# Kernel tuning notes

Hardware: AMD Instinct MI355X
Metric: run time of the kernel (lower is better)

The kernel has to match this reference:

```python
import jax, jax.numpy as jnp
import numpy as np

D_MODEL = 2048
D_STATE = 64
D_HEAD = 64
EXPAND = 2
CHUNK = 256
D_INNER = EXPAND * D_MODEL          # 4096
N_HEADS = D_INNER // D_HEAD          # 64
PARAM_DIM = 1 + 2 * D_STATE          # 129


def setup_inputs() -> dict:
    key = jax.random.key(0)
    k0, k1, k2, k3 = jax.random.split(key, 4)
    x = jax.random.normal(k0, (1, 4096, D_MODEL), jnp.float32)
    w_in = jax.random.normal(k1, (2 * D_INNER, D_MODEL), jnp.float32) * 0.02
    w_param = jax.random.normal(k2, (N_HEADS * PARAM_DIM, D_MODEL), jnp.float32) * 0.02
    w_out = jax.random.normal(k3, (D_MODEL, D_INNER), jnp.float32) * 0.02
    return {"x": x, "w_in": w_in, "w_param": w_param, "w_out": w_out}


def _ssd(a, Bm, Cm, X, Q):
    # a: (nb, l), Bm/Cm: (nb, l, ds), X: (nb, l, dh). Mamba-2 SSD chunked scan.
    nb, l = a.shape
    ds = Bm.shape[-1]
    dh = X.shape[-1]
    nc = l // Q
    la = jnp.log(a).reshape(nb, nc, Q)
    cs = jnp.cumsum(la, axis=-1)                      # cumulative log-decay within chunk
    Bc = Bm.reshape(nb, nc, Q, ds)
    Cc = Cm.reshape(nb, nc, Q, ds)
    Xc = X.reshape(nb, nc, Q, dh)
    # intra-chunk (attention-like dual): L[i,j] = prod_{r=j+1..i} a_r, j<=i
    tri = jnp.tril(jnp.ones((Q, Q), bool))
    L = jnp.where(tri, jnp.exp(cs[..., :, None] - cs[..., None, :]), 0.0)
    scores = jnp.einsum('znid,znjd->znij', Cc, Bc) * L
    y_diag = jnp.einsum('znij,znjh->znih', scores, Xc)
    # per-chunk state contribution: sum_j decay_to_end[j] * B_j^T x_j -> (nb,nc,ds,dh)
    decay_states = jnp.exp(cs[..., -1:] - cs)
    states = jnp.einsum('znj,znjd,znjh->zndh', decay_states, Bc, Xc)
    A_chunk = jnp.exp(cs[..., -1])                    # total decay per chunk (nb, nc)
    def step(S, inp):
        Ac, st = inp
        S_prev = S
        return Ac[:, None, None] * S + st, S_prev
    S0 = jnp.zeros((nb, ds, dh), a.dtype)
    _, S_prev = jax.lax.scan(step, S0, (A_chunk.T, jnp.moveaxis(states, 1, 0)))
    S_prev = jnp.moveaxis(S_prev, 0, 1)               # state entering each chunk (nb,nc,ds,dh)
    y_inter = jnp.einsum('znid,zndh,zni->znih', Cc, S_prev, jnp.exp(cs))
    return (y_diag + y_inter).reshape(nb, l, dh)


def reference(x, w_in, w_param, w_out):
    b, l, _ = x.shape
    xr = x @ w_in.T                                   # (b, l, 2*d_inner)
    inp, res = xr[..., :D_INNER], xr[..., D_INNER:]
    params = (x @ w_param.T).reshape(b, l, N_HEADS, PARAM_DIM)
    dt = jax.nn.softplus(params[..., 0])
    a = jnp.exp(-dt)                                  # (b, l, n_heads)
    Bp = params[..., 1:1 + D_STATE]
    Cp = params[..., 1 + D_STATE:]
    nb = b * N_HEADS
    # NOTE: raw row-major reshapes, mirroring the torch source exactly
    y = _ssd(a.reshape(nb, l),
             Bp.reshape(nb, l, D_STATE),
             Cp.reshape(nb, l, D_STATE),
             inp.reshape(nb, l, D_HEAD),
             CHUNK)
    y = y.reshape(b, l, D_INNER)
    out = y * jax.nn.silu(res)
    return out @ w_out.T
```

## Files before the change

kernel.cpp:

```cpp
#include <hip/hip_runtime.h>
#include <math.h>

#define Q 256

typedef unsigned short u16;
typedef unsigned int u32;
typedef __attribute__((ext_vector_type(8))) short short8;
typedef __attribute__((ext_vector_type(4))) float f32x4;

__device__ __forceinline__ float bf2f(u32 u){
  union { float f; u32 i; } v; v.i = u << 16; return v.f;
}
__device__ __forceinline__ u16 f2bf(float f){
  union { float f; u32 i; } v; v.f = f;
  u32 r = (v.i + 0x7FFFu + ((v.i >> 16) & 1u)) >> 16;
  return (u16)r;
}
__device__ __forceinline__ float softplusf(float x){
  return x > 20.f ? x : log1pf(expf(x));
}
__device__ __forceinline__ float siluf(float x){
  return x / (1.f + expf(-x));
}

__device__ __forceinline__ void gload_lds16(const void* g, const void* l){
  __builtin_amdgcn_global_load_lds(
    (const __attribute__((address_space(1))) void*)(uintptr_t)g,
    (__attribute__((address_space(3))) void*)(u32)(uintptr_t)l,
    16, 0, 0);
}

__device__ __forceinline__ u32 swz_off(int row, int col2){
  return (u32)(row*128 + (col2 ^ ((row & 7) << 4)));
}
__device__ __forceinline__ short8 frag_ld(const u16* buf, int row, int kk, int lk){
  return *(const short8*)((const char*)buf + row*128 + (((kk*4 + lk) ^ (row & 7)) << 4));
}

__global__ __launch_bounds__(256) void cast_bf16(const float* __restrict__ in,
    u16* __restrict__ out)
{
  const size_t i = ((size_t)blockIdx.x * 256 + threadIdx.x) * 4;
  const float4 v = *(const float4*)(in + i);
  ushort4 o;
  o.x = f2bf(v.x); o.y = f2bf(v.y); o.z = f2bf(v.z); o.w = f2bf(v.w);
  *(ushort4*)(out + i) = o;
}

#define G256_VM8 asm volatile("s_waitcnt vmcnt(8)" ::: "memory")
#define G256_VM4 asm volatile("s_waitcnt vmcnt(4)" ::: "memory")
#define G256_VM0 asm volatile("s_waitcnt vmcnt(0)" ::: "memory")

#define G256_STAGE(s_) \
  _Pragma("unroll") for (int q = 0; q < 4; q++) \
    gload_lds16(sptr[q] + (s_)*32, lds + (((s_)&3)*32768) + (q*512 + tid)*16);

#define G256_PHASE(p_, dostage_, VMSTMT) { \
  const char* sb_ = lds + (((p_)&3)*32768); \
  short8 af_[8], bf_[4]; \
  _Pragma("unroll") for (int m = 0; m < 8; m++) af_[m] = *(const short8*)(sb_ + aoff[m]); \
  _Pragma("unroll") for (int n = 0; n < 4; n++) bf_[n] = *(const short8*)(sb_ + boff[n]); \
  if (dostage_) { G256_STAGE((p_)+3) } \
  __builtin_amdgcn_s_barrier(); \
  asm volatile("s_waitcnt lgkmcnt(0)" ::: "memory"); \
  __builtin_amdgcn_sched_barrier(0); \
  __builtin_amdgcn_s_setprio(1); \
  _Pragma("unroll") for (int m = 0; m < 8; m++) \
  _Pragma("unroll") for (int n = 0; n < 4; n++) \
    acc[m][n] = __builtin_amdgcn_mfma_f32_16x16x32_bf16(af_[m], bf_[n], acc[m][n], 0, 0, 0); \
  __builtin_amdgcn_s_setprio(0); \
  VMSTMT; \
  __builtin_amdgcn_s_barrier(); \
}

#define G256_CORE(A_, B_, K_, NTN_) \
  extern __shared__ char lds[]; \
  const int tid = threadIdx.x; \
  const int nwg = gridDim.x, bid = blockIdx.x; \
  const int wg = (bid & 7) * (nwg >> 3) + (bid >> 3); \
  const int m0 = (wg / (NTN_)) * 256, n0 = (wg % (NTN_)) * 256; \
  const int w = tid >> 6, l = tid & 63; \
  const int wr = w >> 2, wc = w & 3; \
  const int lr = l & 15, lk = l >> 4; \
  const u16* sptr[4]; \
  _Pragma("unroll") for (int q = 0; q < 4; q++) { \
    const int c = q*512 + tid; \
    const int r = c >> 3; \
    const int jl = (c & 7) ^ (r & 7); \
    sptr[q] = (jl < 4) ? ((A_) + (size_t)(m0 + r)*(K_) + jl*8) \
                       : ((B_) + (size_t)(n0 + r)*(K_) + (jl-4)*8); \
  } \
  int aoff[8], boff[4]; \
  _Pragma("unroll") for (int m = 0; m < 8; m++) { \
    const int r = wr*128 + m*16 + lr; \
    aoff[m] = r*128 + ((lk ^ (r & 7)) << 4); } \
  _Pragma("unroll") for (int n = 0; n < 4; n++) { \
    const int r = wc*64 + n*16 + lr; \
    boff[n] = r*128 + (((4 + lk) ^ (r & 7)) << 4); } \
  f32x4 acc[8][4]; \
  { f32x4 z = {0.f,0.f,0.f,0.f}; \
    _Pragma("unroll") for (int m = 0; m < 8; m++) \
    _Pragma("unroll") for (int n = 0; n < 4; n++) acc[m][n] = z; } \
  G256_STAGE(0) G256_STAGE(1) G256_STAGE(2) \
  G256_VM8; \
  __builtin_amdgcn_s_barrier(); \
  { const int NPH = (K_)/32; \
    for (int p = 0; p < NPH-4; p += 4) { \
      G256_PHASE(p,   1, G256_VM8) \
      G256_PHASE(p+1, 1, G256_VM8) \
      G256_PHASE(p+2, 1, G256_VM8) \
      G256_PHASE(p+3, 1, G256_VM8) \
    } \
    G256_PHASE(NPH-4, 1, G256_VM8) \
    G256_PHASE(NPH-3, 0, G256_VM4) \
    G256_PHASE(NPH-2, 0, G256_VM0) \
    G256_PHASE(NPH-1, 0, (void)0) \
  }

__global__ void __launch_bounds__(512, 2) gemm_in256(const u16* __restrict__ A,
    const u16* __restrict__ B, u16* __restrict__ inp, u16* __restrict__ resb)
{
  G256_CORE(A, B, 2048, 32)
  #pragma unroll
  for (int m = 0; m < 8; m++)
    #pragma unroll
    for (int n = 0; n < 4; n++) {
      const int col = n0 + wc*64 + n*16 + lr;
      #pragma unroll
      for (int j = 0; j < 4; j++) {
        const int row = m0 + wr*128 + m*16 + lk*4 + j;
        const u16 v = f2bf(acc[m][n][j]);
        if (col < 4096) inp[(size_t)row*4096 + col] = v;
        else            resb[(size_t)row*4096 + (col - 4096)] = v;
      }
    }
}

__global__ void __launch_bounds__(512, 2) gemm_par256(const u16* __restrict__ A,
    const u16* __restrict__ B, float* __restrict__ dtb,
    u16* __restrict__ Bb, u16* __restrict__ Cb)
{
  G256_CORE(A, B, 2048, 33)
  #pragma unroll
  for (int m = 0; m < 8; m++)
    #pragma unroll
    for (int n = 0; n < 4; n++) {
      const int col = n0 + wc*64 + n*16 + lr;
      if (col < 8256) {
        const int h = col / 129, rr = col - h*129;
        #pragma unroll
        for (int j = 0; j < 4; j++) {
          const int row = m0 + wr*128 + m*16 + lk*4 + j;
          const float v = acc[m][n][j];
          if (rr == 0)      dtb[(size_t)row*64 + h] = v;
          else if (rr < 65) Bb[((size_t)row*64 + h)*64 + (rr-1)]  = f2bf(v);
          else              Cb[((size_t)row*64 + h)*64 + (rr-65)] = f2bf(v);
        }
      }
    }
}

#define MFMA_GEMM_CORE(Abf_, Bbf_, K_) \
  __shared__ short As[128*64]; \
  __shared__ short Bs[128*64]; \
  const int tid = threadIdx.x; \
  const int w = tid >> 6, l = tid & 63; \
  const int m0 = blockIdx.y * 128, n0 = blockIdx.x * 128; \
  const int wr = (w >> 1) * 64, wc = (w & 1) * 64; \
  const int sub = l >> 3; \
  const int scol = ((l & 7) ^ sub) * 8; \
  const int lr16 = l & 15; \
  const int koff = (l >> 4) << 4; \
  const int swz = (l & 7) << 4; \
  f32x4 acc[4][4]; \
  { f32x4 z = {0.f, 0.f, 0.f, 0.f}; \
    _Pragma("unroll") for (int m_ = 0; m_ < 4; m_++) \
    _Pragma("unroll") for (int n_ = 0; n_ < 4; n_++) acc[m_][n_] = z; } \
  const u16* Agp = (Abf_) + (size_t)m0 * (K_); \
  const u16* Bgp = (Bbf_) + (size_t)n0 * (K_); \
  for (int kt = 0; kt < (K_); kt += 64) { \
    __syncthreads(); \
    _Pragma("unroll") for (int i_ = 0; i_ < 4; i_++) { \
      const int rbase = i_*32 + w*8; \
      gload_lds16(Agp + (size_t)(rbase + sub)*(K_) + kt + scol, As + rbase*64); \
      gload_lds16(Bgp + (size_t)(rbase + sub)*(K_) + kt + scol, Bs + rbase*64); \
    } \
    __syncthreads(); \
    short8 af[2][4], bf[2][4]; \
    _Pragma("unroll") for (int kk = 0; kk < 2; kk++) { \
      _Pragma("unroll") for (int m_ = 0; m_ < 4; m_++) \
        af[kk][m_] = *(const short8*)((const char*)As + (wr + m_*16 + lr16)*128 + ((kk*64 + koff) ^ swz)); \
      _Pragma("unroll") for (int n_ = 0; n_ < 4; n_++) \
        bf[kk][n_] = *(const short8*)((const char*)Bs + (wc + n_*16 + lr16)*128 + ((kk*64 + koff) ^ swz)); \
    } \
    _Pragma("unroll") for (int m_ = 0; m_ < 4; m_++) \
    _Pragma("unroll") for (int n_ = 0; n_ < 4; n_++) \
    _Pragma("unroll") for (int kk = 0; kk < 2; kk++) \
      acc[m_][n_] = __builtin_amdgcn_mfma_f32_16x16x32_bf16(af[kk][m_], bf[kk][n_], acc[m_][n_], 0, 0, 0); \
  } \
  const int orow0 = m0 + wr + ((l >> 4) << 2); \
  const int ocol0 = n0 + wc + (l & 15);

__global__ __launch_bounds__(256) void gemm_out(const u16* __restrict__ A,
    const u16* __restrict__ B, float* __restrict__ C)
{
  MFMA_GEMM_CORE(A, B, 4096)
  #pragma unroll
  for (int m_ = 0; m_ < 4; m_++)
    #pragma unroll
    for (int n_ = 0; n_ < 4; n_++) {
      const int col = ocol0 + n_*16;
      #pragma unroll
      for (int j = 0; j < 4; j++)
        C[(size_t)(orow0 + m_*16 + j)*2048 + col] = acc[m_][n_][j];
    }
}

__global__ __launch_bounds__(256) void ssd_phaseA(const float* __restrict__ dtb,
    const u16* __restrict__ Bb, const u16* __restrict__ inp,
    float* __restrict__ cs_g, float* __restrict__ achunk, float* __restrict__ states_t)
{
  const int g = blockIdx.x, tid = threadIdx.x;
  const int p = g * Q + tid;
  __shared__ float sc[Q];
  __shared__ u16 sBt[64*64];
  __shared__ u16 sXt[64*64];
  sc[tid] = -softplusf(dtb[p]);
  __syncthreads();
  for (int off = 1; off < Q; off <<= 1) {
    float v = (tid >= off) ? sc[tid - off] : 0.f;
    __syncthreads();
    if (tid >= off) sc[tid] += v;
    __syncthreads();
  }
  cs_g[p] = sc[tid];
  const float cl = sc[Q-1];
  if (tid == 0) achunk[g] = expf(cl);

  const int w = tid >> 6, l = tid & 63;
  const int lrow = l & 15, lk = l >> 4;
  const int tj = tid & 63, tcb = (tid >> 6) * 16;
  f32x4 acc[4];
  { f32x4 z = {0,0,0,0}; acc[0]=z; acc[1]=z; acc[2]=z; acc[3]=z; }

  for (int js = 0; js < 4; js++) {
    __syncthreads();
    {
      const int jc = js*64 + tj;
      const float wj = expf(cl - sc[jc]);
      const size_t prow = ((size_t)g*Q + jc) * 64;
      union { uint4 v; u16 s[8]; } b0, b1, x0, x1;
      b0.v = *(const uint4*)&Bb[prow + tcb];
      b1.v = *(const uint4*)&Bb[prow + tcb + 8];
      x0.v = *(const uint4*)&inp[prow + tcb];
      x1.v = *(const uint4*)&inp[prow + tcb + 8];
      #pragma unroll
      for (int q = 0; q < 8; q++) {
        const int r0 = tcb + q, r1 = tcb + 8 + q;
        *(u16*)((char*)sBt + swz_off(r0, 2*tj)) = f2bf(wj * bf2f((u32)b0.s[q]));
        *(u16*)((char*)sBt + swz_off(r1, 2*tj)) = f2bf(wj * bf2f((u32)b1.s[q]));
        *(u16*)((char*)sXt + swz_off(r0, 2*tj)) = x0.s[q];
        *(u16*)((char*)sXt + swz_off(r1, 2*tj)) = x1.s[q];
      }
    }
    __syncthreads();
    short8 aX0 = frag_ld(sXt, w*16 + lrow, 0, lk);
    short8 aX1 = frag_ld(sXt, w*16 + lrow, 1, lk);
    #pragma unroll
    for (int n = 0; n < 4; n++) {
      short8 b0 = frag_ld(sBt, n*16 + lrow, 0, lk);
      short8 b1 = frag_ld(sBt, n*16 + lrow, 1, lk);
      acc[n] = __builtin_amdgcn_mfma_f32_16x16x32_bf16(aX0, b0, acc[n], 0, 0, 0);
      acc[n] = __builtin_amdgcn_mfma_f32_16x16x32_bf16(aX1, b1, acc[n], 0, 0, 0);
    }
  }
  #pragma unroll
  for (int reg = 0; reg < 4; reg++) {
    const int d = w*16 + lk*4 + reg;
    #pragma unroll
    for (int n = 0; n < 4; n++)
      states_t[(size_t)g*4096 + d*64 + n*16 + lrow] = acc[n][reg];
  }
}

__global__ __launch_bounds__(256) void ssd_scan(float* __restrict__ states,
    const float* __restrict__ achunk)
{
  const int n = blockIdx.x, tid = threadIdx.x;
  float S[16];
  #pragma unroll
  for (int k = 0; k < 16; k++) S[k] = 0.f;
  for (int c = 0; c < 16; c++) {
    const int g = n*16 + c;
    const float A = achunk[g];
    #pragma unroll
    for (int k = 0; k < 16; k++) {
      const size_t e = (size_t)g * 4096 + tid + k*256;
      const float st = states[e];
      states[e] = S[k];
      S[k] = fmaf(A, S[k], st);
    }
  }
}

__global__ __launch_bounds__(256) void ssd_diag(const u16* __restrict__ Bb,
    const u16* __restrict__ Cb, const u16* __restrict__ inp,
    const float* __restrict__ cs_g, const float* __restrict__ states_t,
    const u16* __restrict__ resb, u16* __restrict__ yb)
{
  const int g = blockIdx.y, it = blockIdx.x, tid = threadIdx.x;
  const int w = tid >> 6, l = tid & 63;
  const int lrow = l & 15, lk = l >> 4;
  const int p_base = g * Q;
  __shared__ u16 sC[64*64];
  __shared__ u16 sB[64*64];
  __shared__ u16 sX[64*64];
  __shared__ u16 sP[64*64];
  __shared__ float csi[64], csj[64];

  const int r = tid >> 2, c0 = (tid & 3) << 4;
  {
    const size_t prow = (size_t)(p_base + it*64 + r) * 64;
    uint4 v0 = *(const uint4*)&Cb[prow + c0];
    uint4 v1 = *(const uint4*)&Cb[prow + c0 + 8];
    *(uint4*)((char*)sC + swz_off(r, c0*2))      = v0;
    *(uint4*)((char*)sC + swz_off(r, c0*2 + 16)) = v1;
    if (tid < 64) csi[tid] = cs_g[p_base + it*64 + tid];
  }
  const int i0 = w * 16;
  const int xj = tid & 63, xdb = (tid >> 6) * 16;
  f32x4 accY[4];
  { f32x4 z = {0,0,0,0}; accY[0]=z; accY[1]=z; accY[2]=z; accY[3]=z; }

  for (int jt = 0; jt <= it; jt++) {
    __syncthreads();
    {
      const size_t prow = (size_t)(p_base + jt*64 + r) * 64;
      uint4 v0 = *(const uint4*)&Bb[prow + c0];
      uint4 v1 = *(const uint4*)&Bb[prow + c0 + 8];
      *(uint4*)((char*)sB + swz_off(r, c0*2))      = v0;
      *(uint4*)((char*)sB + swz_off(r, c0*2 + 16)) = v1;
      if (tid < 64) csj[tid] = cs_g[p_base + jt*64 + tid];
    }
    {
      const size_t prow = (size_t)(p_base + jt*64 + xj) * 64;
      union { uint4 v; u16 s[8]; } x0, x1;
      x0.v = *(const uint4*)&inp[prow + xdb];
      x1.v = *(const uint4*)&inp[prow + xdb + 8];
      #pragma unroll
      for (int q = 0; q < 8; q++) {
        *(u16*)((char*)sX + swz_off(xdb + q,     2*xj)) = x0.s[q];
        *(u16*)((char*)sX + swz_off(xdb + 8 + q, 2*xj)) = x1.s[q];
      }
    }
    __syncthreads();
    f32x4 sAcc[4];
    { f32x4 z = {0,0,0,0}; sAcc[0]=z; sAcc[1]=z; sAcc[2]=z; sAcc[3]=z; }
    {
      short8 aC0 = frag_ld(sC, i0 + lrow, 0, lk);
      short8 aC1 = frag_ld(sC, i0 + lrow, 1, lk);
      #pragma unroll
      for (int n = 0; n < 4; n++) {
        short8 b0 = frag_ld(sB, n*16 + lrow, 0, lk);
        short8 b1 = frag_ld(sB, n*16 + lrow, 1, lk);
        sAcc[n] = __builtin_amdgcn_mfma_f32_16x16x32_bf16(aC0, b0, sAcc[n], 0, 0, 0);
        sAcc[n] = __builtin_amdgcn_mfma_f32_16x16x32_bf16(aC1, b1, sAcc[n], 0, 0, 0);
      }
    }
    const bool full = (jt < it);
    #pragma unroll
    for (int n = 0; n < 4; n++) {
      const int j_l = n*16 + lrow;
      const float cj = csj[j_l];
      #pragma unroll
      for (int reg = 0; reg < 4; reg++) {
        const int i_l = i0 + lk*4 + reg;
        float s = 0.f;
        if (full || j_l <= i_l) s = sAcc[n][reg] * expf(csi[i_l] - cj);
        *(u16*)((char*)sP + swz_off(i_l, n*32 + 2*lrow)) = f2bf(s);
      }
    }
    {
      short8 aP0 = frag_ld(sP, i0 + lrow, 0, lk);
      short8 aP1 = frag_ld(sP, i0 + lrow, 1, lk);
      #pragma unroll
      for (int n = 0; n < 4; n++) {
        short8 x0f = frag_ld(sX, n*16 + lrow, 0, lk);
        short8 x1f = frag_ld(sX, n*16 + lrow, 1, lk);
        accY[n] = __builtin_amdgcn_mfma_f32_16x16x32_bf16(aP0, x0f, accY[n], 0, 0, 0);
        accY[n] = __builtin_amdgcn_mfma_f32_16x16x32_bf16(aP1, x1f, accY[n], 0, 0, 0);
      }
    }
  }
  __syncthreads();
  {
    const int d = tid & 63, sb = (tid >> 6) * 16;
    const float* srow = &states_t[(size_t)g*4096 + d*64 + sb];
    float4 f0 = *(const float4*)(srow);
    float4 f1 = *(const float4*)(srow + 4);
    float4 f2 = *(const float4*)(srow + 8);
    float4 f3 = *(const float4*)(srow + 12);
    union { uint4 v; u16 s[8]; } o0, o1;
    o0.s[0]=f2bf(f0.x); o0.s[1]=f2bf(f0.y); o0.s[2]=f2bf(f0.z); o0.s[3]=f2bf(f0.w);
    o0.s[4]=f2bf(f1.x); o0.s[5]=f2bf(f1.y); o0.s[6]=f2bf(f1.z); o0.s[7]=f2bf(f1.w);
    o1.s[0]=f2bf(f2.x); o1.s[1]=f2bf(f2.y); o1.s[2]=f2bf(f2.z); o1.s[3]=f2bf(f2.w);
    o1.s[4]=f2bf(f3.x); o1.s[5]=f2bf(f3.y); o1.s[6]=f2bf(f3.z); o1.s[7]=f2bf(f3.w);
    *(uint4*)((char*)sB + swz_off(d, sb*2))      = o0.v;
    *(uint4*)((char*)sB + swz_off(d, sb*2 + 16)) = o1.v;
  }
  __syncthreads();
  f32x4 accI[4];
  { f32x4 z = {0,0,0,0}; accI[0]=z; accI[1]=z; accI[2]=z; accI[3]=z; }
  {
    short8 aC0 = frag_ld(sC, i0 + lrow, 0, lk);
    short8 aC1 = frag_ld(sC, i0 + lrow, 1, lk);
    #pragma unroll
    for (int n = 0; n < 4; n++) {
      short8 s0 = frag_ld(sB, n*16 + lrow, 0, lk);
      short8 s1 = frag_ld(sB, n*16 + lrow, 1, lk);
      accI[n] = __builtin_amdgcn_mfma_f32_16x16x32_bf16(aC0, s0, accI[n], 0, 0, 0);
      accI[n] = __builtin_amdgcn_mfma_f32_16x16x32_bf16(aC1, s1, accI[n], 0, 0, 0);
    }
  }
  #pragma unroll
  for (int reg = 0; reg < 4; reg++) {
    const int i_l = i0 + lk*4 + reg;
    const float ei = expf(csi[i_l]);
    const size_t prow = (size_t)(p_base + it*64 + i_l) * 64;
    #pragma unroll
    for (int n = 0; n < 4; n++) {
      const int d = n*16 + lrow;
      const float yv = accY[n][reg] + ei * accI[n][reg];
      const float rv = bf2f((u32)resb[prow + d]);
      yb[prow + d] = f2bf(yv * siluf(rv));
    }
  }
}

extern "C" void kernel_launch(void* const* d_in, const int* in_sizes, int n_in,
                              void* d_out, int out_size, void* d_ws, size_t ws_size,
                              hipStream_t stream)
{
  const float* x       = (const float*)d_in[0];
  const float* w_in    = (const float*)d_in[1];
  const float* w_param = (const float*)d_in[2];
  const float* w_out   = (const float*)d_in[3];
  float* out = (float*)d_out;
  char* ws = (char*)d_ws;

  float* states    = (float*)(ws);
  u16*   xb        = (u16*)  (ws);
  u16*   yb        = (u16*)  (ws + 0x1000000ull);
  u16*   w_in_b    = (u16*)  (ws + 0x1000000ull);
  u16*   w_param_b = (u16*)  (ws + 0x3000000ull);
  u16*   w_out_b   = (u16*)  (ws + 0x5100000ull);
  u16*   inp       = (u16*)  (ws + 0x6100000ull);
  u16*   resb      = (u16*)  (ws + 0x8100000ull);
  u16*   Bb        = (u16*)  (ws + 0xA100000ull);
  u16*   Cb        = (u16*)  (ws + 0xC100000ull);
  float* dtb       = (float*)(ws + 0xE100000ull);
  float* cs        = (float*)(ws + 0xE200000ull);
  float* achunk    = (float*)(ws + 0xE300000ull);

  hipFuncSetAttribute((const void*)gemm_in256,
      hipFuncAttributeMaxDynamicSharedMemorySize, 131072);
  hipFuncSetAttribute((const void*)gemm_par256,
      hipFuncAttributeMaxDynamicSharedMemorySize, 131072);

  cast_bf16<<<8192,  256, 0, stream>>>(x, xb);
  cast_bf16<<<16384, 256, 0, stream>>>(w_in, w_in_b);
  cast_bf16<<<16512, 256, 0, stream>>>(w_param, w_param_b);
  cast_bf16<<<8192,  256, 0, stream>>>(w_out, w_out_b);

  gemm_in256 <<<512, 512, 131072, stream>>>(xb, w_in_b, inp, resb);
  gemm_par256<<<528, 512, 131072, stream>>>(xb, w_param_b, dtb, Bb, Cb);
  ssd_phaseA<<<1024, 256, 0, stream>>>(dtb, Bb, inp, cs, achunk, states);
  ssd_scan<<<64, 256, 0, stream>>>(states, achunk);
  ssd_diag<<<dim3(4, 1024), 256, 0, stream>>>(Bb, Cb, inp, cs, states, resb, yb);
  gemm_out<<<dim3(16, 32), 256, 0, stream>>>(yb, w_out_b, out);
}
```

Before: 573.5 us.

## Split GEMM K-step into two half-tile MFMA phases with fewer fragment registers

Restructures the bf16 GEMM main loop so each K-step loads B fragments once and the A fragments in two halves of four. Each half is followed by its own barrier-fenced MFMA block of 16 instructions. The loop becomes a rolled loop with the vmcnt waits chosen at runtime, replacing the unrolled-by-4 phases with their fixed waits. This cuts fragment register pressure and precomputed offsets, and interleaves LDS reads with MFMA. In exchange it doubles the barriers per K-step and puts the stage and wait branches inside the loop.

```diff
diff --git a/kernel.cpp b/kernel.cpp
--- a/kernel.cpp
+++ b/kernel.cpp
@@ -47,33 +47,22 @@
   *(ushort4*)(out + i) = o;
 }
 
-#define G256_VM8 asm volatile("s_waitcnt vmcnt(8)" ::: "memory")
-#define G256_VM4 asm volatile("s_waitcnt vmcnt(4)" ::: "memory")
-#define G256_VM0 asm volatile("s_waitcnt vmcnt(0)" ::: "memory")
-
-#define G256_STAGE(s_) \
+#define G8_STAGE(s_) \
   _Pragma("unroll") for (int q = 0; q < 4; q++) \
     gload_lds16(sptr[q] + (s_)*32, lds + (((s_)&3)*32768) + (q*512 + tid)*16);
 
-#define G256_PHASE(p_, dostage_, VMSTMT) { \
-  const char* sb_ = lds + (((p_)&3)*32768); \
-  short8 af_[8], bf_[4]; \
-  _Pragma("unroll") for (int m = 0; m < 8; m++) af_[m] = *(const short8*)(sb_ + aoff[m]); \
-  _Pragma("unroll") for (int n = 0; n < 4; n++) bf_[n] = *(const short8*)(sb_ + boff[n]); \
-  if (dostage_) { G256_STAGE((p_)+3) } \
+#define G8_MFMA16(mh_) \
   __builtin_amdgcn_s_barrier(); \
   asm volatile("s_waitcnt lgkmcnt(0)" ::: "memory"); \
   __builtin_amdgcn_sched_barrier(0); \
   __builtin_amdgcn_s_setprio(1); \
-  _Pragma("unroll") for (int m = 0; m < 8; m++) \
+  _Pragma("unroll") for (int m = 0; m < 4; m++) \
   _Pragma("unroll") for (int n = 0; n < 4; n++) \
-    acc[m][n] = __builtin_amdgcn_mfma_f32_16x16x32_bf16(af_[m], bf_[n], acc[m][n], 0, 0, 0); \
+    acc[(mh_)*4+m][n] = __builtin_amdgcn_mfma_f32_16x16x32_bf16(aF[m], bF[n], acc[(mh_)*4+m][n], 0, 0, 0); \
   __builtin_amdgcn_s_setprio(0); \
-  VMSTMT; \
-  __builtin_amdgcn_s_barrier(); \
-}
-
-#define G256_CORE(A_, B_, K_, NTN_) \
+  __builtin_amdgcn_s_barrier();
+
+#define G8_CORE(A_, B_, K_, NTN_) \
   extern __shared__ char lds[]; \
   const int tid = threadIdx.x; \
   const int nwg = gridDim.x, bid = blockIdx.x; \
@@ -90,37 +79,40 @@
     sptr[q] = (jl < 4) ? ((A_) + (size_t)(m0 + r)*(K_) + jl*8) \
                        : ((B_) + (size_t)(n0 + r)*(K_) + (jl-4)*8); \
   } \
-  int aoff[8], boff[4]; \
-  _Pragma("unroll") for (int m = 0; m < 8; m++) { \
-    const int r = wr*128 + m*16 + lr; \
-    aoff[m] = r*128 + ((lk ^ (r & 7)) << 4); } \
-  _Pragma("unroll") for (int n = 0; n < 4; n++) { \
-    const int r = wc*64 + n*16 + lr; \
-    boff[n] = r*128 + (((4 + lk) ^ (r & 7)) << 4); } \
+  const int abase0 = (wr*128 + lr)*128 + ((lk ^ (lr & 7)) << 4); \
+  const int bbase0 = (wc*64  + lr)*128 + (((4 + lk) ^ (lr & 7)) << 4); \
   f32x4 acc[8][4]; \
   { f32x4 z = {0.f,0.f,0.f,0.f}; \
     _Pragma("unroll") for (int m = 0; m < 8; m++) \
     _Pragma("unroll") for (int n = 0; n < 4; n++) acc[m][n] = z; } \
-  G256_STAGE(0) G256_STAGE(1) G256_STAGE(2) \
-  G256_VM8; \
+  short8 aF[4], bF[4]; \
+  G8_STAGE(0) G8_STAGE(1) G8_STAGE(2) \
+  asm volatile("s_waitcnt vmcnt(8)" ::: "memory"); \
   __builtin_amdgcn_s_barrier(); \
-  { const int NPH = (K_)/32; \
-    for (int p = 0; p < NPH-4; p += 4) { \
-      G256_PHASE(p,   1, G256_VM8) \
-      G256_PHASE(p+1, 1, G256_VM8) \
-      G256_PHASE(p+2, 1, G256_VM8) \
-      G256_PHASE(p+3, 1, G256_VM8) \
+  { const int NS = (K_)/32; \
+    for (int j = 0; j < NS; ++j) { \
+      const char* sb_ = lds + ((j & 3)*32768); \
+       \
+      if (j < NS-2)       { asm volatile("s_waitcnt vmcnt(8)" ::: "memory"); } \
+      else if (j == NS-2) { asm volatile("s_waitcnt vmcnt(4)" ::: "memory"); } \
+      else                { asm volatile("s_waitcnt vmcnt(0)" ::: "memory"); } \
+      _Pragma("unroll") for (int n = 0; n < 4; n++) \
+        bF[n] = *(const short8*)(sb_ + bbase0 + n*2048); \
+      _Pragma("unroll") for (int m = 0; m < 4; m++) \
+        aF[m] = *(const short8*)(sb_ + abase0 + m*2048); \
+      if (j + 3 < NS) { G8_STAGE(j+3) } \
+      G8_MFMA16(0) \
+       \
+      _Pragma("unroll") for (int m = 0; m < 4; m++) \
+        aF[m] = *(const short8*)(sb_ + abase0 + 8192 + m*2048); \
+      G8_MFMA16(1) \
     } \
-    G256_PHASE(NPH-4, 1, G256_VM8) \
-    G256_PHASE(NPH-3, 0, G256_VM4) \
-    G256_PHASE(NPH-2, 0, G256_VM0) \
-    G256_PHASE(NPH-1, 0, (void)0) \
   }
 
 __global__ void __launch_bounds__(512, 2) gemm_in256(const u16* __restrict__ A,
     const u16* __restrict__ B, u16* __restrict__ inp, u16* __restrict__ resb)
 {
-  G256_CORE(A, B, 2048, 32)
+  G8_CORE(A, B, 2048, 32)
   #pragma unroll
   for (int m = 0; m < 8; m++)
     #pragma unroll
@@ -140,7 +132,7 @@
     const u16* __restrict__ B, float* __restrict__ dtb,
     u16* __restrict__ Bb, u16* __restrict__ Cb)
 {
-  G256_CORE(A, B, 2048, 33)
+  G8_CORE(A, B, 2048, 33)
   #pragma unroll
   for (int m = 0; m < 8; m++)
     #pragma unroll
```

Result: slower. 588.0 us (+2.5%).
